# Kernel tuning notes

Hardware: AMD Instinct MI355X
Metric: run time of the kernel (lower is better)

## Reference

```python
import jax, jax.numpy as jnp
import numpy as np

SAMPLE_RATE = 0.25  # nsample = SAMPLE_RATE * points_num, as in get_indexes


def setup_inputs() -> dict:
    key = jax.random.key(0)
    k1, k2 = jax.random.split(key)
    xyz = jax.random.normal(k1, (32, 16384, 3), dtype=jnp.float32)
    feat = jax.random.normal(k2, (32, 16384, 128), dtype=jnp.float32)
    return {"xyz": xyz, "feat": feat}


def farthest_point_sample(xyz, nsample):
    """Iterative FPS: at each step pick the point farthest from the selected set.
    xyz: [B, N, 3] -> indexes [B, nsample] (int32). Deterministic start at index 0."""
    B, N, _ = xyz.shape

    def step(carry, _):
        dist, farthest = carry  # dist: [B, N] min sq-dist to selected set; farthest: [B]
        centroid = jnp.take_along_axis(xyz, farthest[:, None, None], axis=1)  # [B,1,3]
        d = jnp.sum((xyz - centroid) ** 2, axis=-1)  # [B, N]
        dist = jnp.minimum(dist, d)
        nxt = jnp.argmax(dist, axis=-1).astype(jnp.int32)
        return (dist, nxt), farthest

    init = (jnp.full((B, N), jnp.finfo(xyz.dtype).max, xyz.dtype),
            jnp.zeros((B,), jnp.int32))
    _, idx = jax.lax.scan(step, init, None, length=nsample)  # [nsample, B]
    return idx.T  # [B, nsample]


def index_points(points, idx):
    """points: [B, N, C], idx: [B, S] -> [B, S, C] (torch index_points gather)."""
    return jnp.take_along_axis(points, idx[..., None], axis=1)


def reference(xyz, feat):
    points_num = xyz.shape[1]
    nsample = int(SAMPLE_RATE * points_num)
    sample_indexes = farthest_point_sample(xyz, nsample)  # [B, nsample]
    sampled_xyz = index_points(xyz, sample_indexes)       # [B, nsample, 3]
    sampled_feat = index_points(feat, sample_indexes)     # [B, nsample, C]
    return sampled_xyz, sampled_feat
```

## Files before the change

kernel.cpp:

```cpp
#include <hip/hip_runtime.h>
#include <hip/hip_bf16.h>
#include <cfloat>


#define FPS_THREADS 512

#define REP32(M) M(0) M(1) M(2) M(3) M(4) M(5) M(6) M(7) \
                 M(8) M(9) M(10) M(11) M(12) M(13) M(14) M(15) \
                 M(16) M(17) M(18) M(19) M(20) M(21) M(22) M(23) \
                 M(24) M(25) M(26) M(27) M(28) M(29) M(30) M(31)

__global__ __launch_bounds__(FPS_THREADS, 2)
void fps_kernel(const float* __restrict__ xyz, int* __restrict__ out_idx,
                int N, int S) {
#pragma clang fp contract(off)
  const int b = blockIdx.x;
  const int t = threadIdx.x;
  const float* xb = xyz + (size_t)b * N * 3;

  __shared__ float2 s_xy[16384];
  __shared__ unsigned long long s_k[2][FPS_THREADS / 64];

#define DECLP(k) float pz##k, ds##k;
  REP32(DECLP)

#define LOADP(k) { int p = (k) * FPS_THREADS + t;               \
    s_xy[p] = make_float2(xb[(size_t)p * 3 + 0],                \
                          xb[(size_t)p * 3 + 1]);               \
    pz##k = xb[(size_t)p * 3 + 2];                              \
    ds##k = FLT_MAX; }
  REP32(LOADP)

  const int wave = t >> 6;
  const int lane = t & 63;
  const unsigned invt = 0xFFFFFFFFu - (unsigned)t;
  int farthest = 0;

  __syncthreads();

  for (int s = 0; s < S; ++s) {
    if (t == 0) out_idx[(size_t)b * S + s] = farthest;

    int f = __builtin_amdgcn_readfirstlane(farthest);
    float cz = xb[(size_t)f * 3 + 2];
    float2 cxy = s_xy[f];
    float cx = cxy.x, cy = cxy.y;

    float bestv = -1.0f;
    int bestk = 0;

#define STEPP(k) {                                               \
    float2 xy = s_xy[(k) * FPS_THREADS + t];                     \
    float dx = xy.x - cx;                                        \
    float dy = xy.y - cy;                                        \
    float dz = pz##k - cz;                                       \
    float y2 = dy * dy;                                          \
    float inner = __builtin_fmaf(dx, dx, y2);                    \
    float dd = __builtin_fmaf(dz, dz, inner);                    \
    float nd = fminf(ds##k, dd);                                 \
    ds##k = nd;                                                  \
    if (nd > bestv) { bestv = nd; bestk = (k); } }
    REP32(STEPP)

    unsigned bestinv = invt - (unsigned)(bestk * FPS_THREADS);
    unsigned long long bestkkey =
        ((unsigned long long)__float_as_uint(bestv) << 32) |
        (unsigned long long)bestinv;

#pragma unroll
    for (int off = 32; off > 0; off >>= 1) {
      unsigned long long ok = __shfl_xor(bestkkey, off, 64);
      if (ok > bestkkey) bestkkey = ok;
    }

    const int par = s & 1;
    if (lane == 0) s_k[par][wave] = bestkkey;
    __syncthreads();

    unsigned long long bk = s_k[par][0];
#pragma unroll
    for (int w = 1; w < FPS_THREADS / 64; ++w) {
      unsigned long long ok = s_k[par][w];
      if (ok > bk) bk = ok;
    }
    farthest = (int)(0xFFFFFFFFu - (unsigned)(bk & 0xFFFFFFFFu));
  }
}

__global__ void gather_kernel(const float* __restrict__ xyz,
                              const float* __restrict__ feat,
                              const int* __restrict__ idx,
                              float* __restrict__ out,
                              int B, int N, int S, int C) {
  const int c4pr = C >> 2;
  const int nf4 = B * S * c4pr;
  int tid = blockIdx.x * blockDim.x + threadIdx.x;
  if (tid < nf4) {
    int c4 = tid % c4pr;
    int bs = tid / c4pr;
    int s = bs % S, b = bs / S;
    int p = idx[b * S + s];
    const float4* src = (const float4*)(feat + ((size_t)b * N + p) * C);
    float4* dst = (float4*)(out + (size_t)B * S * 3 + ((size_t)bs) * C);
    dst[c4] = src[c4];
  } else {
    int t2 = tid - nf4;
    int nxyz = B * S * 3;
    if (t2 < nxyz) {
      int c = t2 % 3;
      int bs = t2 / 3;
      int s = bs % S, b = bs / S;
      int p = idx[b * S + s];
      out[t2] = xyz[((size_t)b * N + p) * 3 + c];
    }
  }
}

extern "C" void kernel_launch(void* const* d_in, const int* in_sizes, int n_in,
                              void* d_out, int out_size, void* d_ws, size_t ws_size,
                              hipStream_t stream) {
  const float* xyz = (const float*)d_in[0];
  const float* feat = (const float*)d_in[1];
  float* out = (float*)d_out;

  const int B = 32;
  const int N = in_sizes[0] / (B * 3);
  const int C = in_sizes[1] / (B * N);
  const int S = N / 4;

  int* d_idx = (int*)d_ws;

  fps_kernel<<<B, FPS_THREADS, 0, stream>>>(xyz, d_idx, N, S);

  int total = B * S * (C >> 2) + B * S * 3;
  int blocks = (total + 255) / 256;
  gather_kernel<<<blocks, 256, 0, stream>>>(xyz, feat, d_idx, out, B, N, S, C);
}
```

Baseline: 6.537 ms.

## Stream FPS point coordinates from global SoA buffers instead of LDS/registers

Adds a transpose kernel that splits xyz into separate xy (float2) and z arrays in workspace, and rewrites the FPS loop to read every point's coordinates from global memory (L2/cache) on each iteration instead of keeping xy in shared memory and z in registers. This frees 128KB of LDS and 32 registers per thread. In exchange, each of the 4096 iterations rereads the per-batch point set from the cache hierarchy, which is likely slower than LDS.

```diff
diff --git a/kernel.cpp b/kernel.cpp
--- a/kernel.cpp
+++ b/kernel.cpp
@@ -10,50 +10,60 @@
                  M(16) M(17) M(18) M(19) M(20) M(21) M(22) M(23) \
                  M(24) M(25) M(26) M(27) M(28) M(29) M(30) M(31)
 
+__global__ __launch_bounds__(FPS_THREADS) void transpose_kernel(
+    const float* __restrict__ xyz, float2* __restrict__ xyp,
+    float* __restrict__ zp, int N) {
+  const int b = blockIdx.x;
+  const int t = threadIdx.x;
+  const float* xb = xyz + (size_t)b * N * 3;
+  float2* xyb = xyp + (size_t)b * N;
+  float* zb = zp + (size_t)b * N;
+#pragma unroll
+  for (int k = 0; k < 32; ++k) {
+    int p = k * FPS_THREADS + t;
+    xyb[p] = make_float2(xb[(size_t)p * 3 + 0], xb[(size_t)p * 3 + 1]);
+    zb[p] = xb[(size_t)p * 3 + 2];
+  }
+}
+
 __global__ __launch_bounds__(FPS_THREADS, 2)
-void fps_kernel(const float* __restrict__ xyz, int* __restrict__ out_idx,
-                int N, int S) {
+void fps_kernel(const float2* __restrict__ xyp, const float* __restrict__ zp,
+                int* __restrict__ out_idx, int N, int S) {
 #pragma clang fp contract(off)
   const int b = blockIdx.x;
   const int t = threadIdx.x;
-  const float* xb = xyz + (size_t)b * N * 3;
+  const float2* xyb = xyp + (size_t)b * N;
+  const float* zb = zp + (size_t)b * N;
 
-  __shared__ float2 s_xy[16384];
+#define DECLP(k) float ds##k;
+  REP32(DECLP)
+#define INITP(k) ds##k = FLT_MAX;
+  REP32(INITP)
+
   __shared__ unsigned long long s_k[2][FPS_THREADS / 64];
-
-#define DECLP(k) float pz##k, ds##k;
-  REP32(DECLP)
-
-#define LOADP(k) { int p = (k) * FPS_THREADS + t;               \
-    s_xy[p] = make_float2(xb[(size_t)p * 3 + 0],                \
-                          xb[(size_t)p * 3 + 1]);               \
-    pz##k = xb[(size_t)p * 3 + 2];                              \
-    ds##k = FLT_MAX; }
-  REP32(LOADP)
 
   const int wave = t >> 6;
   const int lane = t & 63;
   const unsigned invt = 0xFFFFFFFFu - (unsigned)t;
   int farthest = 0;
 
-  __syncthreads();
-
   for (int s = 0; s < S; ++s) {
     if (t == 0) out_idx[(size_t)b * S + s] = farthest;
 
     int f = __builtin_amdgcn_readfirstlane(farthest);
-    float cz = xb[(size_t)f * 3 + 2];
-    float2 cxy = s_xy[f];
+    float2 cxy = xyb[f];
+    float cz = zb[f];
     float cx = cxy.x, cy = cxy.y;
 
     float bestv = -1.0f;
     int bestk = 0;
 
 #define STEPP(k) {                                               \
-    float2 xy = s_xy[(k) * FPS_THREADS + t];                     \
+    int p = (k) * FPS_THREADS + t;                               \
+    float2 xy = xyb[p];                                          \
+    float dz = zb[p] - cz;                                       \
     float dx = xy.x - cx;                                        \
     float dy = xy.y - cy;                                        \
-    float dz = pz##k - cz;                                       \
     float y2 = dy * dy;                                          \
     float inner = __builtin_fmaf(dx, dx, y2);                    \
     float dd = __builtin_fmaf(dz, dz, inner);                    \
@@ -129,8 +139,11 @@
   const int S = N / 4;
 
   int* d_idx = (int*)d_ws;
+  float2* d_xy = (float2*)((char*)d_ws + (size_t)B * S * sizeof(int));
+  float* d_z = (float*)((char*)d_xy + (size_t)B * N * sizeof(float2));
 
-  fps_kernel<<<B, FPS_THREADS, 0, stream>>>(xyz, d_idx, N, S);
+  transpose_kernel<<<B, FPS_THREADS, 0, stream>>>(xyz, d_xy, d_z, N);
+  fps_kernel<<<B, FPS_THREADS, 0, stream>>>(d_xy, d_z, d_idx, N, S);
 
   int total = B * S * (C >> 2) + B * S * 3;
   int blocks = (total + 255) / 256;
```

After: 5.979 ms. -8.5%, faster.
